# Kernel optimization log

Measured on AMD Instinct MI355X. Metric: run time of the kernel, lower is better.

## Reference

```python
import jax, jax.numpy as jnp
import numpy as np

B, N_UNITS, SEQ, H = 4, 1024, 2048, 8
D_HEAD = N_UNITS // H
SCALE = 1.0 / D_HEAD ** 0.5


def setup_inputs() -> dict:
    key = jax.random.key(0)
    k1, k2, k3 = jax.random.split(key, 3)
    x = jax.random.normal(k1, (B, N_UNITS, SEQ), dtype=jnp.float32)
    # conv1x1 weights, bias=False; scaled like typical init
    W_qkv = jax.random.normal(k2, (3 * N_UNITS, N_UNITS), dtype=jnp.float32) * (1.0 / N_UNITS ** 0.5)
    W_out = jax.random.normal(k3, (N_UNITS, N_UNITS), dtype=jnp.float32) * (1.0 / N_UNITS ** 0.5)
    return {"x": x, "W_qkv": W_qkv, "W_out": W_out}


def reference(x, W_qkv, W_out):
    # x: (B, n_units, S). Conv1x1 == per-position linear along channel dim.
    qkv = jnp.einsum('oc,bcs->bos', W_qkv, x)          # (B, 3*n_units, S)
    Q, K, V = jnp.split(qkv, 3, axis=1)                # each (B, n_units, S)
    # torch.chunk along channels into h heads == reshape (B, h, d_head, S)
    Q = Q.reshape(B, H, D_HEAD, SEQ)
    K = K.reshape(B, H, D_HEAD, SEQ)
    V = V.reshape(B, H, D_HEAD, SEQ)
    # scores: Q^T K * scale  (NO softmax in original module; mask unused)
    A = jnp.einsum('bhdq,bhdk->bhqk', Q, K) * SCALE    # (B, h, S, S)
    # aggregation: sum_k A[q,k] * V[d,k]  (original does broadcast mul+sum)
    C = jnp.einsum('bhqk,bhdk->bhdq', A, V)            # (B, h, d_head, S)
    C = C.reshape(B, N_UNITS, SEQ)
    out = jnp.einsum('oc,bcs->bos', W_out, C)          # (B, n_units, S)
    return out
```

## Files before the change

kernel.cpp:

```cpp
#include <hip/hip_runtime.h>
#include <hip/hip_bf16.h>
#include <stdint.h>

using bf16 = __hip_bfloat16;

typedef __bf16 bf16x8 __attribute__((ext_vector_type(8)));
typedef float  f32x4  __attribute__((ext_vector_type(4)));

constexpr int Bc = 4, Hh = 8, Dh = 128, S = 2048, Cn = 1024, O3 = 3072;
constexpr float SCALE = 0.08838834764831845f;

#define GLDS16(gp, lp)                                               \
  __builtin_amdgcn_global_load_lds(                                  \
      (const __attribute__((address_space(1))) void*)(gp),           \
      (__attribute__((address_space(3))) void*)(lp), 16, 0, 0)

__device__ __forceinline__ void gemm_bt_core(
    const bf16* __restrict__ Abase, int lda,
    const bf16* __restrict__ Bbase, int ldb,
    int kIters, f32x4 (&acc)[4][4])
{
  alignas(16) __shared__ bf16 As[128 * 32];
  alignas(16) __shared__ bf16 Bs[128 * 32];
  const int t    = threadIdx.x;
  const int lane = t & 63;
  const int quad = lane >> 4, r16 = lane & 15;
  const int wave = t >> 6;
  const int wm = (wave & 1) * 64, wn = (wave >> 1) * 64;
  const int lrow = lane >> 2;
  const int lk   = (lane & 3) * 8;

  const long aOff0 = (long)(wave * 32 + lrow) * lda + lk;
  const long aOff1 = aOff0 + 16l * lda;
  const long bOff0 = (long)(wave * 32 + lrow) * ldb + lk;
  const long bOff1 = bOff0 + 16l * ldb;
  bf16* aL0 = &As[(wave * 32) * 32];
  bf16* aL1 = &As[(wave * 32 + 16) * 32];
  bf16* bL0 = &Bs[(wave * 32) * 32];
  bf16* bL1 = &Bs[(wave * 32 + 16) * 32];

#pragma unroll
  for (int i = 0; i < 4; i++)
#pragma unroll
    for (int j = 0; j < 4; j++) acc[i][j] = {0.f, 0.f, 0.f, 0.f};

  for (int ks = 0; ks < kIters; ++ks) {
    const int k0 = ks * 32;
    __syncthreads();
    GLDS16(Abase + k0 + aOff0, aL0);
    GLDS16(Abase + k0 + aOff1, aL1);
    GLDS16(Bbase + k0 + bOff0, bL0);
    GLDS16(Bbase + k0 + bOff1, bL1);
    __syncthreads();
    bf16x8 af[4], bfr[4];
#pragma unroll
    for (int i = 0; i < 4; i++)
      af[i] = *(const bf16x8*)&As[(wm + i * 16 + r16) * 32 + quad * 8];
#pragma unroll
    for (int j = 0; j < 4; j++)
      bfr[j] = *(const bf16x8*)&Bs[(wn + j * 16 + r16) * 32 + quad * 8];
#pragma unroll
    for (int i = 0; i < 4; i++)
#pragma unroll
      for (int j = 0; j < 4; j++)
        acc[i][j] = __builtin_amdgcn_mfma_f32_16x16x32_bf16(af[i], bfr[j], acc[i][j], 0, 0, 0);
  }
}

__device__ __forceinline__ void store_bf16_tile(
    f32x4 (&acc)[4][4], bf16* __restrict__ Cp, int ldc)
{
  const int t = threadIdx.x;
  const int lane = t & 63;
  const int quad = lane >> 4, r16 = lane & 15;
  const int wave = t >> 6;
  const int wm = (wave & 1) * 64, wn = (wave >> 1) * 64;
#pragma unroll
  for (int i = 0; i < 4; i++)
#pragma unroll
    for (int j = 0; j < 4; j++)
#pragma unroll
      for (int r = 0; r < 4; r++) {
        const int row = wm + i * 16 + quad * 4 + r;
        const int col = wn + j * 16 + r16;
        Cp[(long)row * ldc + col] = __float2bfloat16(acc[i][j][r]);
      }
}

__device__ __forceinline__ void store_f32_tile(
    f32x4 (&acc)[4][4], float* __restrict__ Cp, int ldc)
{
  const int t = threadIdx.x;
  const int lane = t & 63;
  const int quad = lane >> 4, r16 = lane & 15;
  const int wave = t >> 6;
  const int wm = (wave & 1) * 64, wn = (wave >> 1) * 64;
#pragma unroll
  for (int i = 0; i < 4; i++)
#pragma unroll
    for (int j = 0; j < 4; j++)
#pragma unroll
      for (int r = 0; r < 4; r++) {
        const int row = wm + i * 16 + quad * 4 + r;
        const int col = wn + j * 16 + r16;
        Cp[(long)row * ldc + col] = acc[i][j][r];
      }
}

__global__ __launch_bounds__(256) void k_cvt_w(
    const float* __restrict__ Wkv, const float* __restrict__ Wout,
    bf16* __restrict__ WkvB, bf16* __restrict__ WoutB)
{
  const long v = (long)blockIdx.x * 256 + threadIdx.x;
  const bool isK = v < 524288;
  const float4 f = isK ? ((const float4*)Wkv)[v] : ((const float4*)Wout)[v - 524288];
  bf16 tmp[4];
  tmp[0] = __float2bfloat16(f.x);
  tmp[1] = __float2bfloat16(f.y);
  tmp[2] = __float2bfloat16(f.z);
  tmp[3] = __float2bfloat16(f.w);
  ushort4 u = *(ushort4*)tmp;
  if (isK) ((ushort4*)WkvB)[v] = u;
  else     ((ushort4*)WoutB)[v - 524288] = u;
}

__global__ __launch_bounds__(256) void k_transpose_cvt(
    const float* __restrict__ in, bf16* __restrict__ out, long inZ, long outZ,
    int inld, int outld)
{
  __shared__ bf16 tile[32][33];
  const float* ip = in + (long)blockIdx.z * inZ;
  bf16* op = out + (long)blockIdx.z * outZ;
  const int c0 = blockIdx.x * 32, r0 = blockIdx.y * 32;
  const int tx = threadIdx.x & 31, ty = threadIdx.x >> 5;
#pragma unroll
  for (int i = 0; i < 32; i += 8)
    tile[ty + i][tx] = __float2bfloat16(ip[(long)(r0 + ty + i) * inld + c0 + tx]);
  __syncthreads();
#pragma unroll
  for (int i = 0; i < 32; i += 8)
    op[(long)(c0 + ty + i) * outld + r0 + tx] = tile[tx][ty + i];
}

__global__ __launch_bounds__(256) void k_gemm_kv(
    const bf16* __restrict__ WkvB, const bf16* __restrict__ xT, bf16* __restrict__ KV)
{
  const int m0 = blockIdx.x * 128, n0 = blockIdx.y * 128, b = blockIdx.z;
  f32x4 acc[4][4];
  gemm_bt_core(WkvB + (long)m0 * Cn, Cn,
               xT + (long)b * S * Cn + (long)n0 * Cn, Cn, Cn / 32, acc);
  store_bf16_tile(acc, KV + (long)b * 2048 * S + (long)m0 * S + n0, S);
}

__global__ __launch_bounds__(256) void k_gemm_mt(
    const bf16* __restrict__ KV, float* __restrict__ MTpart)
{
  const int chunk = blockIdx.x;
  const int z = blockIdx.y;
  const int b = z >> 3, h = z & 7;
  const bf16* base = KV + (long)b * 2048 * S;
  const bf16* A  = base + (long)(h * Dh) * S + chunk * 256;
  const bf16* Bp = base + (long)(1024 + h * Dh) * S + chunk * 256;
  f32x4 acc[4][4];
  gemm_bt_core(A, S, Bp, S, 8, acc);
  store_f32_tile(acc, MTpart + ((long)chunk * 32 + z) * (Dh * Dh), Dh);
}

__global__ __launch_bounds__(256) void k_reduce_mt(
    const float* __restrict__ MTpart, bf16* __restrict__ MbT)
{
  const long i = (long)blockIdx.x * 256 + threadIdx.x;
  float s = 0.f;
#pragma unroll
  for (int c = 0; c < 8; c++) s += MTpart[(long)c * 32 * Dh * Dh + i];
  MbT[i] = __float2bfloat16(s * SCALE);
}

__global__ __launch_bounds__(256) void k_gemm_w2(
    const bf16* __restrict__ WoutB, const bf16* __restrict__ MbT, bf16* __restrict__ W2)
{
  const int m0 = blockIdx.x * 128;
  const int h = blockIdx.y, b = blockIdx.z;
  const int z = b * 8 + h;
  f32x4 acc[4][4];
  gemm_bt_core(WoutB + (long)m0 * Cn + h * Dh, Cn,
               MbT + (long)z * Dh * Dh, Dh, 4, acc);
  store_bf16_tile(acc, W2 + (long)b * Cn * Cn + (long)m0 * Cn + h * Dh, Cn);
}

__global__ __launch_bounds__(256) void k_gemm_w3(
    const bf16* __restrict__ W2, const bf16* __restrict__ WqT, bf16* __restrict__ W3)
{
  const int m0 = blockIdx.x * 128, n0 = blockIdx.y * 128, b = blockIdx.z;
  f32x4 acc[4][4];
  gemm_bt_core(W2 + (long)b * Cn * Cn + (long)m0 * Cn, Cn,
               WqT + (long)n0 * Cn, Cn, Cn / 32, acc);
  store_bf16_tile(acc, W3 + (long)b * Cn * Cn + (long)m0 * Cn + n0, Cn);
}

__global__ __launch_bounds__(256) void k_gemm_out(
    const bf16* __restrict__ W3, const bf16* __restrict__ xT, float* __restrict__ out)
{
  const int m0 = blockIdx.x * 128, n0 = blockIdx.y * 128, b = blockIdx.z;
  f32x4 acc[4][4];
  gemm_bt_core(W3 + (long)b * Cn * Cn + (long)m0 * Cn, Cn,
               xT + (long)b * S * Cn + (long)n0 * Cn, Cn, Cn / 32, acc);
  store_f32_tile(acc, out + (long)b * Cn * S + (long)m0 * S + n0, S);
}

extern "C" void kernel_launch(void* const* d_in, const int* in_sizes, int n_in,
                              void* d_out, int out_size, void* d_ws, size_t ws_size,
                              hipStream_t stream)
{
  const float* x    = (const float*)d_in[0];
  const float* Wqkv = (const float*)d_in[1];
  const float* Wout = (const float*)d_in[2];
  float* out = (float*)d_out;

  char* ws = (char*)d_ws;
  bf16*  KV     = (bf16*)ws;
  bf16*  xT     = (bf16*)(ws + 33554432);
  float* MTpart = (float*)(ws + 50331648);
  bf16*  W3     = (bf16*)(ws + 50331648);
  bf16*  WkvB   = (bf16*)(ws + 67108864);
  bf16*  WoutB  = (bf16*)(ws + 71303168);
  bf16*  WqT    = (bf16*)(ws + 73400320);
  bf16*  MbT    = (bf16*)(ws + 75497472);
  bf16*  W2     = (bf16*)(ws + 76546048);

  k_cvt_w<<<dim3(3072), 256, 0, stream>>>(Wqkv + (long)Cn * Cn, Wout, WkvB, WoutB);
  k_transpose_cvt<<<dim3(64, 32, 4), 256, 0, stream>>>(
      x, xT, (long)1024 * 2048, (long)2048 * 1024, 2048, 1024);
  k_transpose_cvt<<<dim3(32, 32, 1), 256, 0, stream>>>(
      Wqkv, WqT, 0, 0, 1024, 1024);
  k_gemm_kv<<<dim3(16, 16, 4), 256, 0, stream>>>(WkvB, xT, KV);
  k_gemm_mt<<<dim3(8, 32), 256, 0, stream>>>(KV, MTpart);
  k_reduce_mt<<<dim3(2048), 256, 0, stream>>>(MTpart, MbT);
  k_gemm_w2<<<dim3(8, 8, 4), 256, 0, stream>>>(WoutB, MbT, W2);
  k_gemm_w3<<<dim3(8, 8, 4), 256, 0, stream>>>(W2, WqT, W3);
  k_gemm_out<<<dim3(8, 16, 4), 256, 0, stream>>>(W3, xT, out);
}
```

Measured before the change: 219.9 us.

## Replace KV projection GEMM with 256x256 multi-stage pipelined 8-wave kernel

Swaps the 128x128 single-buffered KV projection GEMM for a 256x256 tile kernel with 8 waves, a 4-slot LDS ring with three stages of global-to-LDS loads in flight, XOR-swizzled LDS layout, grid swizzle for L2 locality, and s_setprio around MFMA bursts. The aim is to hide global load latency behind MFMA work and cut LDS bank conflicts and redundant tile loads in the largest GEMM. The hand-written vmcnt waits and barriers are fragile, and the 128 KB of LDS per block limits occupancy.

```diff
diff --git a/kernel.cpp b/kernel.cpp
--- a/kernel.cpp
+++ b/kernel.cpp
@@ -14,6 +14,14 @@
   __builtin_amdgcn_global_load_lds(                                  \
       (const __attribute__((address_space(1))) void*)(gp),           \
       (__attribute__((address_space(3))) void*)(lp), 16, 0, 0)
+
+#define WAITVM(N) asm volatile("s_waitcnt vmcnt(" #N ")" ::: "memory")
+#define BAR()                                  \
+  do {                                         \
+    asm volatile("" ::: "memory");             \
+    __builtin_amdgcn_s_barrier();              \
+    asm volatile("" ::: "memory");             \
+  } while (0)
 
 __device__ __forceinline__ void gemm_bt_core(
     const bf16* __restrict__ Abase, int lda,
@@ -105,6 +113,114 @@
         const int col = wn + j * 16 + r16;
         Cp[(long)row * ldc + col] = acc[i][j][r];
       }
+}
+
+__global__ __launch_bounds__(512, 2) void k_gemm_kv8(
+    const bf16* __restrict__ WkvB, const bf16* __restrict__ xT, bf16* __restrict__ KV)
+{
+  constexpr int NT = Cn / 32;
+  alignas(16) __shared__ bf16 smem[4 * 16384];
+
+  const int orig = blockIdx.x;
+  const int swz  = (orig & 7) * 32 + (orig >> 3);
+  const int mt = swz >> 5;
+  const int nt = swz & 31;
+  const int m0 = mt * 256;
+
+  const int tid  = threadIdx.x;
+  const int lane = tid & 63;
+  const int w    = tid >> 6;
+  const int quad = lane >> 4, r16 = lane & 15;
+  const int wm = (w >> 2) * 128;
+  const int wn = (w & 3) * 64;
+
+  const int srow = w * 16 + (lane >> 2);
+  const int cx   = (lane & 3) ^ ((lane >> 3) & 3);
+  const bf16* Ag = WkvB + (long)(m0 + srow) * Cn + cx * 8;
+  const bf16* Bg = xT + (long)((long)nt * 256 + srow) * Cn + cx * 8;
+  const int ldsW = w * 512;
+
+#define KV8_STAGE_A(tt)                                                   \
+  do {                                                                    \
+    const int k0_ = (tt) * 32, bb_ = ((tt) & 3) * 16384;                  \
+    GLDS16(Ag + k0_,            &smem[bb_ + ldsW]);                       \
+    GLDS16(Ag + 128l * Cn + k0_, &smem[bb_ + 4096 + ldsW]);               \
+  } while (0)
+#define KV8_STAGE_B(tt)                                                   \
+  do {                                                                    \
+    const int k0_ = (tt) * 32, bb_ = ((tt) & 3) * 16384;                  \
+    GLDS16(Bg + k0_,            &smem[bb_ + 8192 + ldsW]);                \
+    GLDS16(Bg + 128l * Cn + k0_, &smem[bb_ + 8192 + 4096 + ldsW]);        \
+  } while (0)
+
+  const int sc8 = (quad ^ ((r16 >> 1) & 3)) * 8;
+
+  f32x4 acc[8][4];
+#pragma unroll
+  for (int m = 0; m < 8; m++)
+#pragma unroll
+    for (int n = 0; n < 4; n++) acc[m][n] = {0.f, 0.f, 0.f, 0.f};
+
+  KV8_STAGE_A(0); KV8_STAGE_B(0);
+  KV8_STAGE_A(1); KV8_STAGE_B(1);
+  KV8_STAGE_A(2); KV8_STAGE_B(2);
+  WAITVM(8);
+  BAR();
+
+#pragma unroll 2
+  for (int tt = 0; tt < NT; ++tt) {
+    const bf16* Ab = &smem[(tt & 3) * 16384];
+    const bf16* Bb = Ab + 8192;
+    bf16x8 af[4], bfr[4];
+
+#pragma unroll
+    for (int n = 0; n < 4; n++)
+      bfr[n] = *(const bf16x8*)&Bb[(wn + n * 16 + r16) * 32 + sc8];
+#pragma unroll
+    for (int m = 0; m < 4; m++)
+      af[m] = *(const bf16x8*)&Ab[(wm + m * 16 + r16) * 32 + sc8];
+    if (tt + 3 < NT) KV8_STAGE_A(tt + 3);
+    BAR();
+    __builtin_amdgcn_s_setprio(1);
+#pragma unroll
+    for (int m = 0; m < 4; m++)
+#pragma unroll
+      for (int n = 0; n < 4; n++)
+        acc[m][n] = __builtin_amdgcn_mfma_f32_16x16x32_bf16(af[m], bfr[n], acc[m][n], 0, 0, 0);
+    __builtin_amdgcn_s_setprio(0);
+    BAR();
+
+#pragma unroll
+    for (int m = 0; m < 4; m++)
+      af[m] = *(const bf16x8*)&Ab[(wm + (m + 4) * 16 + r16) * 32 + sc8];
+    if (tt + 3 < NT) KV8_STAGE_B(tt + 3);
+    if (tt <= NT - 4)      { WAITVM(8); }
+    else if (tt == NT - 3) { WAITVM(4); }
+    else if (tt == NT - 2) { WAITVM(0); }
+    BAR();
+    __builtin_amdgcn_s_setprio(1);
+#pragma unroll
+    for (int m = 0; m < 4; m++)
+#pragma unroll
+      for (int n = 0; n < 4; n++)
+        acc[m + 4][n] = __builtin_amdgcn_mfma_f32_16x16x32_bf16(af[m], bfr[n], acc[m + 4][n], 0, 0, 0);
+    __builtin_amdgcn_s_setprio(0);
+    BAR();
+  }
+
+  bf16* Cp = KV + (long)(nt >> 3) * 2048 * S + (long)m0 * S + (nt & 7) * 256;
+#pragma unroll
+  for (int m = 0; m < 8; m++)
+#pragma unroll
+    for (int n = 0; n < 4; n++)
+#pragma unroll
+      for (int r = 0; r < 4; r++) {
+        const int row = wm + m * 16 + quad * 4 + r;
+        const int col = wn + n * 16 + r16;
+        Cp[(long)row * S + col] = __float2bfloat16(acc[m][n][r]);
+      }
+#undef KV8_STAGE_A
+#undef KV8_STAGE_B
 }
 
 __global__ __launch_bounds__(256) void k_cvt_w(
@@ -142,16 +258,6 @@
     op[(long)(c0 + ty + i) * outld + r0 + tx] = tile[tx][ty + i];
 }
 
-__global__ __launch_bounds__(256) void k_gemm_kv(
-    const bf16* __restrict__ WkvB, const bf16* __restrict__ xT, bf16* __restrict__ KV)
-{
-  const int m0 = blockIdx.x * 128, n0 = blockIdx.y * 128, b = blockIdx.z;
-  f32x4 acc[4][4];
-  gemm_bt_core(WkvB + (long)m0 * Cn, Cn,
-               xT + (long)b * S * Cn + (long)n0 * Cn, Cn, Cn / 32, acc);
-  store_bf16_tile(acc, KV + (long)b * 2048 * S + (long)m0 * S + n0, S);
-}
-
 __global__ __launch_bounds__(256) void k_gemm_mt(
     const bf16* __restrict__ KV, float* __restrict__ MTpart)
 {
@@ -233,7 +339,7 @@
       x, xT, (long)1024 * 2048, (long)2048 * 1024, 2048, 1024);
   k_transpose_cvt<<<dim3(32, 32, 1), 256, 0, stream>>>(
       Wqkv, WqT, 0, 0, 1024, 1024);
-  k_gemm_kv<<<dim3(16, 16, 4), 256, 0, stream>>>(WkvB, xT, KV);
+  k_gemm_kv8<<<dim3(256), 512, 0, stream>>>(WkvB, xT, KV);
   k_gemm_mt<<<dim3(8, 32), 256, 0, stream>>>(KV, MTpart);
   k_reduce_mt<<<dim3(2048), 256, 0, stream>>>(MTpart, MbT);
   k_gemm_w2<<<dim3(8, 8, 4), 256, 0, stream>>>(WoutB, MbT, W2);
```

Result: faster. 213.3 us (-3.0%).
